# Optimization experiments

Hardware: AMD Instinct MI355X
Metric: run time of the kernel (lower is better)

The kernel has to match this reference:

```python
import jax, jax.numpy as jnp
import numpy as np

B = 128          # batch of codewords
M_CHK = 288      # n_check_nodes
N_VAR = 576      # n_variable_nodes
K_INFO = 288     # n_information_bits
N_ITER = 5
EDGE_P = 0.02    # ~11-12 edges per check row, LDPC-like sparsity


def setup_inputs() -> dict:
    key = jax.random.key(0)
    k1, k2, k3, k4 = jax.random.split(key, 4)
    inputs = jax.random.normal(k1, (B, N_VAR), dtype=jnp.float32)
    # sparse binary parity-check matrix, batched (keras RNN constants carry batch dim)
    H = jax.random.bernoulli(k2, EDGE_P, (B, M_CHK, N_VAR)).astype(jnp.float32)
    sigma2 = 0.5 + 0.5 * jax.random.uniform(k3, (B, 1), dtype=jnp.float32)
    # learned parameters
    input_ponderation = jnp.ones((N_ITER, 1), dtype=jnp.float32)
    out_ponderation = jnp.ones((N_ITER, 1), dtype=jnp.float32)
    skip_ponderation = jnp.ones((1, 1), dtype=jnp.float32)
    # per-edge check-to-variable weights of the neural BP cell
    w_cv = 1.0 + 0.02 * jax.random.normal(k4, (M_CHK, N_VAR), dtype=jnp.float32)
    gate_logit = jnp.asarray(0.0, dtype=jnp.float32)
    return {"inputs": inputs, "H": H, "sigma2": sigma2,
            "input_ponderation": input_ponderation,
            "out_ponderation": out_ponderation,
            "skip_ponderation": skip_ponderation,
            "w_cv": w_cv, "gate_logit": gate_logit}


def _decode(inputs, H, sigma2, input_ponderation, out_ponderation,
            skip_ponderation, w_cv, gate_logit):
    llrs = -4.0 * inputs / sigma2                                    # [B, n]
    # trainable=True path: normalize by mean |llr|
    norm_llrs = llrs / jnp.mean(jnp.abs(llrs), axis=-1, keepdims=True)
    # tile over iterations and apply input ponderation -> [B, T, n]
    x = norm_llrs[:, None, :] * input_ponderation

    mask = H                                                         # [B, m, n]
    gate = jax.nn.sigmoid(gate_logit)

    def cell(Mstate, x_t):
        # variable-to-check extrinsic messages on edges
        S = jnp.sum(Mstate, axis=1, keepdims=True)                   # [B, 1, n]
        V = (x_t[:, None, :] + S - Mstate) * mask                    # [B, m, n]
        # tanh-product check-node update (product excluding self via divide)
        t = jnp.tanh(0.5 * jnp.clip(V, -15.0, 15.0))
        t_edge = jnp.where(mask > 0, t, 1.0)
        P = jnp.prod(t_edge, axis=-1, keepdims=True)                 # [B, m, 1]
        t_safe = jnp.where(jnp.abs(t_edge) < 1e-7,
                           jnp.where(t_edge >= 0, 1e-7, -1e-7), t_edge)
        r = jnp.clip(P / t_safe, -1.0 + 1e-6, 1.0 - 1e-6)
        M_new = 2.0 * jnp.arctanh(r) * w_cv * mask                   # weighted c2v
        # gated (damped) state update
        M_out = gate * M_new + (1.0 - gate) * Mstate
        posterior = x_t + jnp.sum(M_out, axis=1)                     # [B, n]
        return M_out, posterior

    M0 = jnp.zeros_like(H)
    xs = jnp.swapaxes(x, 0, 1)                                       # [T, B, n]
    _, posts = jax.lax.scan(cell, M0, xs)
    outputs = jnp.swapaxes(posts, 0, 1)                              # [B, T, n]

    # post-normalization per iteration, weighted pooling over iterations
    norm_out = outputs / jnp.mean(jnp.abs(outputs), axis=-1, keepdims=True)
    pooled = jnp.mean(out_ponderation * norm_out, axis=-2)           # [B, n]
    out = pooled + skip_ponderation * norm_llrs                      # [1,1] broadcast
    return jax.nn.sigmoid(-out[:, :K_INFO])


def reference(inputs, H, sigma2, input_ponderation, out_ponderation,
              skip_ponderation, w_cv, gate_logit):
    return _decode(inputs, H, sigma2, input_ponderation, out_ponderation,
                   skip_ponderation, w_cv, gate_logit)
```

## Files before the change

### kernel.cpp

```cpp
#include <hip/hip_runtime.h>

#define B_SZ 128
#define MCHK 288
#define NVAR 576
#define KINFO 288
#define NITER 5
#define CAP 40
#define LCAP 3712
#define TPB 1024
#define EPT 4

__global__ __launch_bounds__(TPB) void decode(
    const float* __restrict__ inp,   const float* __restrict__ H,
    const float* __restrict__ sigma2,
    const float* __restrict__ ipond, const float* __restrict__ opond,
    const float* __restrict__ skipp, const float* __restrict__ wcv,
    const float* __restrict__ gatel, float* __restrict__ out) {

    __shared__ __align__(16) float MT[(MCHK * CAP) / 2];
    __shared__ unsigned int ev[LCAP];
    __shared__ float xln[NVAR];
    __shared__ float S[NVAR];
    __shared__ float pooled[NVAR];
    __shared__ float Prow[MCHK];
    __shared__ int   rcnt[MCHK];
    __shared__ int   roff[MCHK];
    __shared__ float red[16];
    __shared__ int   wsumI[16];
    __shared__ int   EtotS;

    float* const tld = MT;
    unsigned short* const stage = (unsigned short*)MT;

    const int b    = blockIdx.x;
    const int tid  = threadIdx.x;
    const int wid  = tid >> 6;
    const int lane = tid & 63;

    const float sig  = sigma2[b];
    const float gate = 1.0f / (1.0f + __expf(-gatel[0]));
    const float gbar = 1.0f - gate;
    const float skip = skipp[0];

    float ipl[NITER], opl[NITER];
    #pragma unroll
    for (int t = 0; t < NITER; ++t) { ipl[t] = ipond[t]; opl[t] = opond[t]; }

    float l = 0.0f;
    if (tid < NVAR) l = -4.0f * inp[(size_t)b * NVAR + tid] / sig;
    float al = (tid < NVAR) ? fabsf(l) : 0.0f;
    #pragma unroll
    for (int o = 32; o; o >>= 1) al += __shfl_down(al, o, 64);
    if (lane == 0) red[wid] = al;

    {
        const float* Hb = H + (size_t)b * (MCHK * NVAR);
        const float* hr0 = Hb + (size_t)wid * NVAR;
        float4 a  = ((const float4*)hr0)[lane];
        float4 bq = ((const float4*)hr0)[64 + lane];
        float  hc = hr0[512 + lane];
        for (int m = wid; m < MCHK; m += 16) {
            const int mn = m + 16;
            float4 na = a, nbq = bq; float nhc = hc;
            if (mn < MCHK) {
                const float* hr = Hb + (size_t)mn * NVAR;
                na  = ((const float4*)hr)[lane];
                nbq = ((const float4*)hr)[64 + lane];
                nhc = hr[512 + lane];
            }
            int cnt = (a.x!=0.f)+(a.y!=0.f)+(a.z!=0.f)+(a.w!=0.f)
                    + (bq.x!=0.f)+(bq.y!=0.f)+(bq.z!=0.f)+(bq.w!=0.f) + (hc!=0.f);
            int pre = cnt;
            #pragma unroll
            for (int o = 1; o < 64; o <<= 1) {
                int n = __shfl_up(pre, o, 64);
                if (lane >= o) pre += n;
            }
            int p = pre - cnt;
            unsigned short* dst = stage + m * CAP;
            int base = lane * 4;
            if (a.x!=0.f)  { if (p<CAP) dst[p] = (unsigned short)(base    ); p++; }
            if (a.y!=0.f)  { if (p<CAP) dst[p] = (unsigned short)(base + 1); p++; }
            if (a.z!=0.f)  { if (p<CAP) dst[p] = (unsigned short)(base + 2); p++; }
            if (a.w!=0.f)  { if (p<CAP) dst[p] = (unsigned short)(base + 3); p++; }
            if (bq.x!=0.f) { if (p<CAP) dst[p] = (unsigned short)(256 + base    ); p++; }
            if (bq.y!=0.f) { if (p<CAP) dst[p] = (unsigned short)(256 + base + 1); p++; }
            if (bq.z!=0.f) { if (p<CAP) dst[p] = (unsigned short)(256 + base + 2); p++; }
            if (bq.w!=0.f) { if (p<CAP) dst[p] = (unsigned short)(256 + base + 3); p++; }
            if (hc!=0.f)   { if (p<CAP) dst[p] = (unsigned short)(512 + lane);     p++; }
            if (lane == 63) rcnt[m] = (pre > CAP) ? CAP : pre;
            a = na; bq = nbq; hc = nhc;
        }
    }
    __syncthreads();

    int myc = 0, incl = 0;
    if (tid < 320) {
        myc  = (tid < MCHK) ? rcnt[tid] : 0;
        incl = myc;
        #pragma unroll
        for (int o = 1; o < 64; o <<= 1) {
            int n = __shfl_up(incl, o, 64);
            if (lane >= o) incl += n;
        }
        if (lane == 63) wsumI[wid] = incl;
    }
    __syncthreads();
    if (tid < MCHK) {
        int o = incl - myc;
        #pragma unroll
        for (int w = 0; w < 4; ++w) if (w < wid) o += wsumI[w];
        int c = myc;
        if (o >= LCAP)         { o = 0; c = 0; }
        else if (o + c > LCAP) { c = LCAP - o; }
        roff[tid] = o; rcnt[tid] = c;
        const unsigned short* sg = stage + tid * CAP;
        for (int j = 0; j < c; ++j)
            ev[o + j] = ((unsigned)tid << 16) | (unsigned)sg[j];
    }
    if (tid < NVAR) { S[tid] = 0.0f; pooled[tid] = 0.0f; }
    if (tid == 0) {
        int e = wsumI[0] + wsumI[1] + wsumI[2] + wsumI[3] + wsumI[4];
        EtotS = (e > LCAP) ? LCAP : e;
    }
    __syncthreads();
    const int E = EtotS;

    {
        float s = 0.0f;
        #pragma unroll
        for (int i = 0; i < 16; ++i) s += red[i];
        const float sc = (float)NVAR / s;
        if (tid < NVAR) xln[tid] = l * sc;
    }
    unsigned evr[EPT]; float wre[EPT], Ml[EPT], tre[EPT];
    #pragma unroll
    for (int k = 0; k < EPT; ++k) {
        evr[k] = 0u; wre[k] = 0.0f; Ml[k] = 0.0f; tre[k] = 0.0f;
        const int e = tid + k * TPB;
        if (e < E) {
            const unsigned pk = ev[e];
            evr[k] = pk;
            wre[k] = wcv[(pk >> 16) * NVAR + (pk & 0xFFFFu)];
        }
    }
    __syncthreads();

    for (int t = 0; t < NITER; ++t) {
        const float pt = ipl[t], ot = opl[t];

        #pragma unroll
        for (int k = 0; k < EPT; ++k) {
            const int e = tid + k * TPB;
            if (e < E) {
                const int v = (int)(evr[k] & 0xFFFFu);
                float V = fmaf(pt, xln[v], S[v]) - Ml[k];
                V = fminf(15.0f, fmaxf(-15.0f, V));
                float ex = __expf(V);
                float te = (ex - 1.0f) * __builtin_amdgcn_rcpf(ex + 1.0f);
                float x  = 0.5f * V, x2 = x * x;
                float tp = x * fmaf(x2, fmaf(x2, fmaf(x2, -0.05396825f, 0.13333333f),
                                             -0.33333333f), 1.0f);
                const float tv = (fabsf(V) < 0.5f) ? tp : te;
                tre[k] = tv;
                tld[e] = tv;
            }
        }
        __syncthreads();

        if (tid < MCHK) {
            const int c = rcnt[tid], o = roff[tid];
            float P = 1.0f;
            if (c > 0) {
                float cur = tld[o];
                for (int j = 1; j < c; ++j) {
                    const float nx = tld[o + j];
                    P *= cur;
                    cur = nx;
                }
                P *= cur;
            }
            Prow[tid] = P;
        }
        if (tid < NVAR) S[tid] = 0.0f;
        __syncthreads();

        #pragma unroll
        for (int k = 0; k < EPT; ++k) {
            const int e = tid + k * TPB;
            if (e < E) {
                const unsigned pk = evr[k];
                const int v = (int)(pk & 0xFFFFu);
                const int m = (int)(pk >> 16);
                const float tj = tre[k];
                const float ts = (fabsf(tj) < 1e-7f) ? ((tj >= 0.0f) ? 1e-7f : -1e-7f) : tj;
                float r = Prow[m] * __builtin_amdgcn_rcpf(ts);
                r = fminf(1.0f - 1e-6f, fmaxf(-1.0f + 1e-6f, r));
                const float Mn = __logf((1.0f + r) * __builtin_amdgcn_rcpf(1.0f - r)) * wre[k];
                const float Mo = fmaf(gate, Mn, gbar * Ml[k]);
                Ml[k] = Mo;
                atomicAdd(&S[v], Mo);
            }
        }
        __syncthreads();

        float post = 0.0f, ap = 0.0f;
        if (tid < NVAR) { post = fmaf(pt, xln[tid], S[tid]); ap = fabsf(post); }
        #pragma unroll
        for (int o = 32; o; o >>= 1) ap += __shfl_down(ap, o, 64);
        if (lane == 0) red[wid] = ap;
        __syncthreads();
        float s2 = 0.0f;
        #pragma unroll
        for (int i = 0; i < 16; ++i) s2 += red[i];
        if (tid < NVAR) pooled[tid] += ot * post * ((float)NVAR / s2);
    }

    if (tid < KINFO) {
        float o = pooled[tid] * (1.0f / NITER) + skip * xln[tid];
        out[(size_t)b * KINFO + tid] = 1.0f / (1.0f + __expf(o));
    }
}

extern "C" void kernel_launch(void* const* d_in, const int* in_sizes, int n_in,
                              void* d_out, int out_size, void* d_ws, size_t ws_size,
                              hipStream_t stream) {
    const float* inp    = (const float*)d_in[0];
    const float* H      = (const float*)d_in[1];
    const float* sigma2 = (const float*)d_in[2];
    const float* ipond  = (const float*)d_in[3];
    const float* opond  = (const float*)d_in[4];
    const float* skipp  = (const float*)d_in[5];
    const float* wcv    = (const float*)d_in[6];
    const float* gatel  = (const float*)d_in[7];
    float* out = (float*)d_out;

    decode<<<B_SZ, TPB, 0, stream>>>(inp, H, sigma2, ipond, opond, skipp,
                                     wcv, gatel, out);
}
```

Baseline: 170.5 us.

## Split H edge extraction into a wide pre-pass kernel and defer per-iteration normalization

```diff
diff --git a/kernel.cpp b/kernel.cpp
--- a/kernel.cpp
+++ b/kernel.cpp
@@ -10,9 +10,42 @@
 #define TPB 1024
 #define EPT 4
 
+__device__ __align__(16) unsigned short g_idx[(size_t)B_SZ * MCHK * CAP];
+__device__ int g_cnt[B_SZ * MCHK];
+
+__global__ __launch_bounds__(256) void build_edges(const float* __restrict__ H) {
+    const int row  = blockIdx.x * 4 + (threadIdx.x >> 6);
+    const int lane = threadIdx.x & 63;
+    const float* hrow = H + (size_t)row * NVAR;
+    const float4* h4  = (const float4*)hrow;
+    float4 a  = h4[lane];
+    float4 bq = h4[64 + lane];
+    float  c  = hrow[512 + lane];
+    int cnt = (a.x!=0.f)+(a.y!=0.f)+(a.z!=0.f)+(a.w!=0.f)
+            + (bq.x!=0.f)+(bq.y!=0.f)+(bq.z!=0.f)+(bq.w!=0.f) + (c!=0.f);
+    int pre = cnt;
+    #pragma unroll
+    for (int o = 1; o < 64; o <<= 1) {
+        int n = __shfl_up(pre, o, 64);
+        if (lane >= o) pre += n;
+    }
+    int p = pre - cnt;
+    unsigned short* dst = g_idx + (size_t)row * CAP;
+    int base = lane * 4;
+    if (a.x!=0.f)  { if (p<CAP) dst[p] = (unsigned short)(base    ); p++; }
+    if (a.y!=0.f)  { if (p<CAP) dst[p] = (unsigned short)(base + 1); p++; }
+    if (a.z!=0.f)  { if (p<CAP) dst[p] = (unsigned short)(base + 2); p++; }
+    if (a.w!=0.f)  { if (p<CAP) dst[p] = (unsigned short)(base + 3); p++; }
+    if (bq.x!=0.f) { if (p<CAP) dst[p] = (unsigned short)(256 + base    ); p++; }
+    if (bq.y!=0.f) { if (p<CAP) dst[p] = (unsigned short)(256 + base + 1); p++; }
+    if (bq.z!=0.f) { if (p<CAP) dst[p] = (unsigned short)(256 + base + 2); p++; }
+    if (bq.w!=0.f) { if (p<CAP) dst[p] = (unsigned short)(256 + base + 3); p++; }
+    if (c!=0.f)    { if (p<CAP) dst[p] = (unsigned short)(512 + lane);     p++; }
+    if (lane == 63) g_cnt[row] = (pre > CAP) ? CAP : pre;
+}
+
 __global__ __launch_bounds__(TPB) void decode(
-    const float* __restrict__ inp,   const float* __restrict__ H,
-    const float* __restrict__ sigma2,
+    const float* __restrict__ inp,   const float* __restrict__ sigma2,
     const float* __restrict__ ipond, const float* __restrict__ opond,
     const float* __restrict__ skipp, const float* __restrict__ wcv,
     const float* __restrict__ gatel, float* __restrict__ out) {
@@ -21,11 +54,11 @@
     __shared__ unsigned int ev[LCAP];
     __shared__ float xln[NVAR];
     __shared__ float S[NVAR];
-    __shared__ float pooled[NVAR];
     __shared__ float Prow[MCHK];
     __shared__ int   rcnt[MCHK];
     __shared__ int   roff[MCHK];
     __shared__ float red[16];
+    __shared__ float redT[NITER][16];
     __shared__ int   wsumI[16];
     __shared__ int   EtotS;
 
@@ -53,43 +86,15 @@
     for (int o = 32; o; o >>= 1) al += __shfl_down(al, o, 64);
     if (lane == 0) red[wid] = al;
 
+    if (tid < MCHK) rcnt[tid] = g_cnt[b * MCHK + tid];
     {
-        const float* Hb = H + (size_t)b * (MCHK * NVAR);
-        const float* hr0 = Hb + (size_t)wid * NVAR;
-        float4 a  = ((const float4*)hr0)[lane];
-        float4 bq = ((const float4*)hr0)[64 + lane];
-        float  hc = hr0[512 + lane];
-        for (int m = wid; m < MCHK; m += 16) {
-            const int mn = m + 16;
-            float4 na = a, nbq = bq; float nhc = hc;
-            if (mn < MCHK) {
-                const float* hr = Hb + (size_t)mn * NVAR;
-                na  = ((const float4*)hr)[lane];
-                nbq = ((const float4*)hr)[64 + lane];
-                nhc = hr[512 + lane];
-            }
-            int cnt = (a.x!=0.f)+(a.y!=0.f)+(a.z!=0.f)+(a.w!=0.f)
-                    + (bq.x!=0.f)+(bq.y!=0.f)+(bq.z!=0.f)+(bq.w!=0.f) + (hc!=0.f);
-            int pre = cnt;
-            #pragma unroll
-            for (int o = 1; o < 64; o <<= 1) {
-                int n = __shfl_up(pre, o, 64);
-                if (lane >= o) pre += n;
-            }
-            int p = pre - cnt;
-            unsigned short* dst = stage + m * CAP;
-            int base = lane * 4;
-            if (a.x!=0.f)  { if (p<CAP) dst[p] = (unsigned short)(base    ); p++; }
-            if (a.y!=0.f)  { if (p<CAP) dst[p] = (unsigned short)(base + 1); p++; }
-            if (a.z!=0.f)  { if (p<CAP) dst[p] = (unsigned short)(base + 2); p++; }
-            if (a.w!=0.f)  { if (p<CAP) dst[p] = (unsigned short)(base + 3); p++; }
-            if (bq.x!=0.f) { if (p<CAP) dst[p] = (unsigned short)(256 + base    ); p++; }
-            if (bq.y!=0.f) { if (p<CAP) dst[p] = (unsigned short)(256 + base + 1); p++; }
-            if (bq.z!=0.f) { if (p<CAP) dst[p] = (unsigned short)(256 + base + 2); p++; }
-            if (bq.w!=0.f) { if (p<CAP) dst[p] = (unsigned short)(256 + base + 3); p++; }
-            if (hc!=0.f)   { if (p<CAP) dst[p] = (unsigned short)(512 + lane);     p++; }
-            if (lane == 63) rcnt[m] = (pre > CAP) ? CAP : pre;
-            a = na; bq = nbq; hc = nhc;
+        const uint4* src = (const uint4*)(g_idx + (size_t)b * (MCHK * CAP));
+        uint4* dst = (uint4*)stage;
+        const int n16 = (MCHK * CAP * 2) / 16;
+        #pragma unroll
+        for (int i = 0; i < 2; ++i) {
+            const int j = tid + i * TPB;
+            if (j < n16) dst[j] = src[j];
         }
     }
     __syncthreads();
@@ -118,7 +123,7 @@
         for (int j = 0; j < c; ++j)
             ev[o + j] = ((unsigned)tid << 16) | (unsigned)sg[j];
     }
-    if (tid < NVAR) { S[tid] = 0.0f; pooled[tid] = 0.0f; }
+    if (tid < NVAR) S[tid] = 0.0f;
     if (tid == 0) {
         int e = wsumI[0] + wsumI[1] + wsumI[2] + wsumI[3] + wsumI[4];
         EtotS = (e > LCAP) ? LCAP : e;
@@ -146,8 +151,13 @@
     }
     __syncthreads();
 
+    float p[NITER];
+    #pragma unroll
+    for (int t = 0; t < NITER; ++t) { p[t] = 0.0f; }
+
+    #pragma unroll
     for (int t = 0; t < NITER; ++t) {
-        const float pt = ipl[t], ot = opl[t];
+        const float pt = ipl[t];
 
         #pragma unroll
         for (int k = 0; k < EPT; ++k) {
@@ -182,7 +192,10 @@
             }
             Prow[tid] = P;
         }
-        if (tid < NVAR) S[tid] = 0.0f;
+        if (tid < NVAR) {
+            if (t > 0) p[t - 1] = fmaf(ipl[t - 1], xln[tid], S[tid]);
+            S[tid] = 0.0f;
+        }
         __syncthreads();
 
         #pragma unroll
@@ -203,21 +216,29 @@
             }
         }
         __syncthreads();
-
-        float post = 0.0f, ap = 0.0f;
-        if (tid < NVAR) { post = fmaf(pt, xln[tid], S[tid]); ap = fabsf(post); }
+    }
+
+    if (tid < NVAR) p[NITER - 1] = fmaf(ipl[NITER - 1], xln[tid], S[tid]);
+
+    #pragma unroll
+    for (int t = 0; t < NITER; ++t) {
+        float ap = (tid < NVAR) ? fabsf(p[t]) : 0.0f;
         #pragma unroll
         for (int o = 32; o; o >>= 1) ap += __shfl_down(ap, o, 64);
-        if (lane == 0) red[wid] = ap;
-        __syncthreads();
-        float s2 = 0.0f;
-        #pragma unroll
-        for (int i = 0; i < 16; ++i) s2 += red[i];
-        if (tid < NVAR) pooled[tid] += ot * post * ((float)NVAR / s2);
-    }
+        if (lane == 0) redT[t][wid] = ap;
+    }
+    __syncthreads();
 
     if (tid < KINFO) {
-        float o = pooled[tid] * (1.0f / NITER) + skip * xln[tid];
+        float pooled = 0.0f;
+        #pragma unroll
+        for (int t = 0; t < NITER; ++t) {
+            float s2 = 0.0f;
+            #pragma unroll
+            for (int i = 0; i < 16; ++i) s2 += redT[t][i];
+            pooled += opl[t] * p[t] * ((float)NVAR / s2);
+        }
+        float o = pooled * (1.0f / NITER) + skip * xln[tid];
         out[(size_t)b * KINFO + tid] = 1.0f / (1.0f + __expf(o));
     }
 }
@@ -235,6 +256,7 @@
     const float* gatel  = (const float*)d_in[7];
     float* out = (float*)d_out;
 
-    decode<<<B_SZ, TPB, 0, stream>>>(inp, H, sigma2, ipond, opond, skipp,
+    build_edges<<<(B_SZ * MCHK) / 4, 256, 0, stream>>>(H);
+    decode<<<B_SZ, TPB, 0, stream>>>(inp, sigma2, ipond, opond, skipp,
                                      wcv, gatel, out);
 }
```

After: 172.7 us. About the same (+1.3%).
